# Performance work log

Hardware: AMD Instinct MI355X
Metric: run time of the kernel (lower is better)

The kernel has to match this reference:

```python
import jax, jax.numpy as jnp
import numpy as np

N_NODES = 100000
N_EDGES = 1600000
IN_CH = 128
OUT_CH = 128
BN_EPS = 1e-5


def setup_inputs() -> dict:
    key = jax.random.key(0)
    ks = jax.random.split(key, 8)
    x = jax.random.normal(ks[0], (N_NODES, IN_CH), dtype=jnp.float32)
    edge_index = jax.random.randint(ks[1], (2, N_EDGES), 0, N_NODES, dtype=jnp.int32)
    s1 = 1.0 / np.sqrt(IN_CH)
    s2 = 1.0 / np.sqrt(OUT_CH)
    W1 = jax.random.uniform(ks[2], (IN_CH, OUT_CH), minval=-s1, maxval=s1, dtype=jnp.float32)
    b1 = jax.random.uniform(ks[3], (OUT_CH,), minval=-s1, maxval=s1, dtype=jnp.float32)
    gamma = jnp.ones((OUT_CH,), dtype=jnp.float32)
    beta = jnp.zeros((OUT_CH,), dtype=jnp.float32)
    W2 = jax.random.uniform(ks[4], (OUT_CH, OUT_CH), minval=-s2, maxval=s2, dtype=jnp.float32)
    b2 = jax.random.uniform(ks[5], (OUT_CH,), minval=-s2, maxval=s2, dtype=jnp.float32)
    return {"x": x, "edge_index": edge_index, "W1": W1, "b1": b1,
            "gamma": gamma, "beta": beta, "W2": W2, "b2": b2}


def reference(x, edge_index, W1, b1, gamma, beta, W2, b2):
    # GINConv (eps=0): h_i = x_i + sum_{(j->i) in E} x_j
    src, dst = edge_index[0], edge_index[1]
    agg = jax.ops.segment_sum(x[src], dst, num_segments=N_NODES)  # [N, in_ch]
    h = x + agg
    # MLP: Linear -> BatchNorm1d (training-mode batch stats) -> ReLU -> Linear -> ReLU
    h = h @ W1 + b1                                   # [N, out_ch]
    mean = jnp.mean(h, axis=0)
    var = jnp.mean(jnp.square(h - mean), axis=0)      # biased variance, as in BN training
    h = (h - mean) * jax.lax.rsqrt(var + BN_EPS) * gamma + beta
    h = jax.nn.relu(h)
    h = h @ W2 + b2
    return jax.nn.relu(h)
```

## Files before the change

kernel.cpp:

```cpp
#include <hip/hip_runtime.h>
#include <hip/hip_bf16.h>
#include <hip/hip_fp16.h>
#include <stdint.h>

#define CH 128
#define NCHUNK 512
#define MAXBKT 2048

typedef _Float16 f16x8 __attribute__((ext_vector_type(8)));
typedef float f32x4 __attribute__((ext_vector_type(4)));

static __device__ __forceinline__ float4 ld4(const float* p) {
    return *reinterpret_cast<const float4*>(p);
}

static __device__ __forceinline__ void cvt_store_fp16(uint32_t* xh, int i, float4 v0, float4 v1) {
    __half2 h0 = __floats2half2_rn(v0.x, v0.y);
    __half2 h1 = __floats2half2_rn(v0.z, v0.w);
    __half2 h2 = __floats2half2_rn(v1.x, v1.y);
    __half2 h3 = __floats2half2_rn(v1.z, v1.w);
    uint4 o;
    o.x = *reinterpret_cast<unsigned*>(&h0);
    o.y = *reinterpret_cast<unsigned*>(&h1);
    o.z = *reinterpret_cast<unsigned*>(&h2);
    o.w = *reinterpret_cast<unsigned*>(&h3);
    reinterpret_cast<uint4*>(xh)[i] = o;
}

__global__ __launch_bounds__(256) void k_bhist_cvt(const float* __restrict__ x,
        uint32_t* __restrict__ xh, int n8, const int* __restrict__ dst,
        int* __restrict__ H, int nE, int nbkt, int chunkSz) {
    __shared__ int hist[MAXBKT];
    int c = blockIdx.x, tid = threadIdx.x;
    int gsz = gridDim.x * 256;
    for (int i = c * 256 + tid; i < n8; i += gsz)
        cvt_store_fp16(xh, i, ld4(x + (size_t)i * 8), ld4(x + (size_t)i * 8 + 4));
    for (int i = tid; i < nbkt; i += 256) hist[i] = 0;
    __syncthreads();
    int s = c * chunkSz, e = min(s + chunkSz, nE);
    for (int i = s + tid; i < e; i += 256) atomicAdd(&hist[dst[i] >> 6], 1);
    __syncthreads();
    for (int i = tid; i < nbkt; i += 256) H[c * nbkt + i] = hist[i];
}

__global__ void k_btot(const int* __restrict__ H, int* __restrict__ T, int nchunk, int nbkt) {
    __shared__ int sd[256];
    int b = blockIdx.x, tid = threadIdx.x;
    int v = 0;
    for (int c = tid; c < nchunk; c += 256) v += H[c * nbkt + b];
    sd[tid] = v;
    __syncthreads();
    for (int o = 128; o > 0; o >>= 1) {
        if (tid < o) sd[tid] += sd[tid + o];
        __syncthreads();
    }
    if (tid == 0) T[b] = sd[0];
}

__global__ __launch_bounds__(1024) void k_bscan(const int* __restrict__ T,
                                                int* __restrict__ base, int nbkt) {
    __shared__ int ps[1024];
    int t = threadIdx.x;
    int a0 = (2 * t < nbkt) ? T[2 * t] : 0;
    int a1 = (2 * t + 1 < nbkt) ? T[2 * t + 1] : 0;
    ps[t] = a0 + a1;
    __syncthreads();
    for (int d = 1; d < 1024; d <<= 1) {
        int v = (t >= d) ? ps[t - d] : 0;
        __syncthreads();
        ps[t] += v;
        __syncthreads();
    }
    int excl = t ? ps[t - 1] : 0;
    if (2 * t < nbkt) base[2 * t] = excl;
    if (2 * t + 1 < nbkt) base[2 * t + 1] = excl + a0;
    if (t == 0) base[nbkt] = ps[1023];
}

__global__ __launch_bounds__(512) void k_boff(int* H, const int* __restrict__ base,
                                              int nchunk, int nbkt) {
    __shared__ int sd[NCHUNK];
    int b = blockIdx.x, t = threadIdx.x;
    int v = (t < nchunk) ? H[t * nbkt + b] : 0;
    sd[t] = v;
    __syncthreads();
    for (int d = 1; d < NCHUNK; d <<= 1) {
        int tv = (t >= d) ? sd[t - d] : 0;
        __syncthreads();
        sd[t] += tv;
        __syncthreads();
    }
    if (t < nchunk) H[t * nbkt + b] = base[b] + sd[t] - v;
}

__global__ void k_bscatter(const int* __restrict__ src, const int* __restrict__ dst,
                           const int* __restrict__ H, int* __restrict__ sorted,
                           int nE, int nbkt, int chunkSz) {
    __shared__ int cur[MAXBKT];
    int c = blockIdx.x, tid = threadIdx.x;
    for (int i = tid; i < nbkt; i += 256) cur[i] = H[c * nbkt + i];
    __syncthreads();
    int s = c * chunkSz, e = min(s + chunkSz, nE);
    for (int i = s + tid; i < e; i += 256) {
        int d = dst[i];
        int pos = atomicAdd(&cur[d >> 6], 1);
        sorted[pos] = src[i] | ((d & 63) << 17);
    }
}

__global__ __launch_bounds__(256) void k_bsort2(const int* __restrict__ sorted,
        const int* __restrict__ base, int* __restrict__ csr, int* __restrict__ offs,
        int n, int nbkt, int nE) {
    __shared__ int hist[64];
    __shared__ int cur[64];
    int b = blockIdx.x, tid = threadIdx.x;
    if (tid < 64) hist[tid] = 0;
    __syncthreads();
    int s = base[b], e = base[b + 1];
    for (int i = s + tid; i < e; i += 256)
        atomicAdd(&hist[(sorted[i] >> 17) & 63], 1);
    __syncthreads();
    if (tid < 64) {
        int h0 = hist[tid], v = h0;
        for (int d = 1; d < 64; d <<= 1) {
            int t = __shfl_up(v, d, 64);
            if (tid >= d) v += t;
        }
        int excl = base[b] + v - h0;
        int node = b * 64 + tid;
        if (node < n) offs[node] = excl;
        cur[tid] = excl;
    }
    if (b == 0 && tid == 0) offs[n] = nE;
    __syncthreads();
    for (int i = s + tid; i < e; i += 256) {
        int p = sorted[i];
        int pos = atomicAdd(&cur[(p >> 17) & 63], 1);
        csr[pos] = (p & 0x1FFFF) << 5;
    }
}

static __device__ __forceinline__ void acc4(float4& a, uint2 v) {
    __half2 p0 = *reinterpret_cast<__half2*>(&v.x);
    __half2 p1 = *reinterpret_cast<__half2*>(&v.y);
    float2 f0 = __half22float2(p0), f1 = __half22float2(p1);
    a.x += f0.x; a.y += f0.y; a.z += f1.x; a.w += f1.y;
}

__global__ void k_aggregate_h2(const uint2* __restrict__ xv,
        const int* __restrict__ csr, const int* __restrict__ offs,
        uint2* __restrict__ h16, int n) {
    int wid = (blockIdx.x * blockDim.x + threadIdx.x) >> 6;
    int lane = threadIdx.x & 63;
    int nw = (gridDim.x * blockDim.x) >> 6;
    int hf = lane >> 5;
    int l32 = lane & 31;
    for (int node = wid; node < n; node += nw) {
        float4 a0 = make_float4(0.f, 0.f, 0.f, 0.f), a1 = a0, a2 = a0, a3 = a0;
        if (hf == 0) acc4(a0, xv[(size_t)node * 32 + l32]);
        int s = offs[node], e = offs[node + 1];
        int i = s + hf;
        for (; i + 14 < e; i += 16) {
            uint2 v0 = xv[csr[i]      + l32];
            uint2 v1 = xv[csr[i + 2]  + l32];
            uint2 v2 = xv[csr[i + 4]  + l32];
            uint2 v3 = xv[csr[i + 6]  + l32];
            uint2 v4 = xv[csr[i + 8]  + l32];
            uint2 v5 = xv[csr[i + 10] + l32];
            uint2 v6 = xv[csr[i + 12] + l32];
            uint2 v7 = xv[csr[i + 14] + l32];
            acc4(a0, v0); acc4(a1, v1); acc4(a2, v2); acc4(a3, v3);
            acc4(a0, v4); acc4(a1, v5); acc4(a2, v6); acc4(a3, v7);
        }
        for (; i + 6 < e; i += 8) {
            uint2 v0 = xv[csr[i]     + l32];
            uint2 v1 = xv[csr[i + 2] + l32];
            uint2 v2 = xv[csr[i + 4] + l32];
            uint2 v3 = xv[csr[i + 6] + l32];
            acc4(a0, v0); acc4(a1, v1); acc4(a2, v2); acc4(a3, v3);
        }
        for (; i < e; i += 2)
            acc4(a0, xv[csr[i] + l32]);
        a0.x += a1.x + a2.x + a3.x;
        a0.y += a1.y + a2.y + a3.y;
        a0.z += a1.z + a2.z + a3.z;
        a0.w += a1.w + a2.w + a3.w;
        a0.x += __shfl_xor(a0.x, 32, 64);
        a0.y += __shfl_xor(a0.y, 32, 64);
        a0.z += __shfl_xor(a0.z, 32, 64);
        a0.w += __shfl_xor(a0.w, 32, 64);
        if (hf == 0) {
            __half2 o0 = __floats2half2_rn(a0.x, a0.y);
            __half2 o1 = __floats2half2_rn(a0.z, a0.w);
            unsigned long long ov =
                (unsigned long long)(*reinterpret_cast<unsigned*>(&o0)) |
                ((unsigned long long)(*reinterpret_cast<unsigned*>(&o1)) << 32);
            __builtin_nontemporal_store(ov,
                reinterpret_cast<unsigned long long*>(&h16[(size_t)node * 32 + l32]));
        }
    }
}

__global__ __launch_bounds__(256) void k_mgemm(
        const _Float16* __restrict__ A, const float* __restrict__ W,
        const float* __restrict__ bias, _Float16* __restrict__ O16,
        float* __restrict__ O32, float* __restrict__ statsOut,
        const float* __restrict__ statsIn, const float* __restrict__ gamma,
        const float* __restrict__ beta, float invN, int nrows, int doStats) {
    __shared__ _Float16 WT[CH * CH];
    __shared__ float sc_sh[2 * CH];
    int tid = threadIdx.x;
    for (int idx4 = tid * 4; idx4 < CH * CH; idx4 += 1024) {
        float4 wv = ld4(W + idx4);
        int k = idx4 >> 7, col = idx4 & 127;
        int s = k >> 3, j = k & 7;
#pragma unroll
        for (int q = 0; q < 4; ++q) {
            int c = col + q;
            WT[c * CH + ((s ^ (c & 7)) << 3) + j] =
                (_Float16)(q == 0 ? wv.x : q == 1 ? wv.y : q == 2 ? wv.z : wv.w);
        }
    }
    if (statsIn && tid < CH) {
        float mean = statsIn[tid] * invN;
        float var = statsIn[CH + tid] * invN - mean * mean;
        float sc = gamma[tid] * rsqrtf(var + 1e-5f);
        sc_sh[tid] = sc;
        sc_sh[CH + tid] = beta[tid] - mean * sc;
    }
    __syncthreads();

    int wv = tid >> 6, lane = tid & 63;
    int lr = lane & 15;
    int lg = lane >> 4;

    float bv[8];
#pragma unroll
    for (int ct = 0; ct < 8; ++ct) bv[ct] = bias[ct * 16 + lr];
    float ssum[8], ssq[8];
#pragma unroll
    for (int ct = 0; ct < 8; ++ct) { ssum[ct] = 0.f; ssq[ct] = 0.f; }

    int nchunks = (nrows + 63) >> 6;
    for (int chunk = blockIdx.x; chunk < nchunks; chunk += gridDim.x) {
        int row0 = chunk * 64 + wv * 16;
        int arow = min(row0 + lr, nrows - 1);
        const _Float16* Ap = A + (size_t)arow * CH + lg * 8;
        f16x8 a[4];
#pragma unroll
        for (int kb = 0; kb < 4; ++kb)
            a[kb] = *reinterpret_cast<const f16x8*>(Ap + kb * 32);
        if (statsIn) {
#pragma unroll
            for (int kb = 0; kb < 4; ++kb) {
                int k0 = kb * 32 + lg * 8;
#pragma unroll
                for (int j = 0; j < 8; ++j) {
                    float f = (float)a[kb][j];
                    f = fmaxf(fmaf(f, sc_sh[k0 + j], sc_sh[CH + k0 + j]), 0.f);
                    a[kb][j] = (_Float16)f;
                }
            }
        }

        f32x4 acc[8];
#pragma unroll
        for (int ct = 0; ct < 8; ++ct) acc[ct] = (f32x4){0.f, 0.f, 0.f, 0.f};
#pragma unroll
        for (int ct = 0; ct < 8; ++ct) {
            int col = ct * 16 + lr;
            const _Float16* Wp = &WT[col * CH];
            int sw = (col & 7) << 3;
#pragma unroll
            for (int kb = 0; kb < 4; ++kb) {
                int s = kb * 4 + lg;
                f16x8 b = *reinterpret_cast<const f16x8*>(Wp + ((s << 3) ^ sw));
                acc[ct] = __builtin_amdgcn_mfma_f32_16x16x32_f16(a[kb], b, acc[ct], 0, 0, 0);
            }
        }

#pragma unroll
        for (int ct = 0; ct < 8; ++ct) {
            int col = ct * 16 + lr;
#pragma unroll
            for (int r = 0; r < 4; ++r) {
                int row = row0 + lg * 4 + r;
                if (row < nrows) {
                    float v = acc[ct][r] + bv[ct];
                    if (doStats) {
                        O16[(size_t)row * CH + col] = (_Float16)v;
                        ssum[ct] += v;
                        ssq[ct] += v * v;
                    } else {
                        O32[(size_t)row * CH + col] = fmaxf(v, 0.f);
                    }
                }
            }
        }
    }

    if (doStats) {
#pragma unroll
        for (int ct = 0; ct < 8; ++ct) {
            ssum[ct] += __shfl_xor(ssum[ct], 16, 64); ssum[ct] += __shfl_xor(ssum[ct], 32, 64);
            ssq[ct]  += __shfl_xor(ssq[ct], 16, 64);  ssq[ct]  += __shfl_xor(ssq[ct], 32, 64);
        }
        __syncthreads();
        float* red = (float*)WT;
        if (lg == 0) {
#pragma unroll
            for (int ct = 0; ct < 8; ++ct) {
                red[wv * 128 + ct * 16 + lr] = ssum[ct];
                red[512 + wv * 128 + ct * 16 + lr] = ssq[ct];
            }
        }
        __syncthreads();
        if (tid < 128) {
            float s = 0.f, q = 0.f;
#pragma unroll
            for (int w = 0; w < 4; ++w) { s += red[w * 128 + tid]; q += red[512 + w * 128 + tid]; }
            atomicAdd(&statsOut[tid], s);
            atomicAdd(&statsOut[128 + tid], q);
        }
    }
}

extern "C" void kernel_launch(void* const* d_in, const int* in_sizes, int n_in,
                              void* d_out, int out_size, void* d_ws, size_t ws_size,
                              hipStream_t stream) {
    const float* x     = (const float*)d_in[0];
    const int*   ei    = (const int*)d_in[1];
    const float* W1    = (const float*)d_in[2];
    const float* b1    = (const float*)d_in[3];
    const float* gamma = (const float*)d_in[4];
    const float* beta  = (const float*)d_in[5];
    const float* W2    = (const float*)d_in[6];
    const float* b2    = (const float*)d_in[7];

    int N = in_sizes[0] / CH;
    int E = in_sizes[1] / 2;
    const int* esrc = ei;
    const int* edst = ei + E;
    int nbkt = (N + 63) >> 6;
    int chunkSz = (E + NCHUNK - 1) / NCHUNK;
    int n8 = N * CH / 8;

    int* H      = (int*)d_out;
    int* sorted = (int*)((char*)d_out + (((size_t)NCHUNK * nbkt * 4 + 255) & ~(size_t)255));
    _Float16* h16 = (_Float16*)d_out;

    char* w = (char*)d_ws;
    auto take = [&](size_t bytes) {
        char* p = w;
        w += (bytes + 255) & ~(size_t)255;
        return p;
    };
    int*      csr    = (int*)take((size_t)E * 4);
    int*      T      = (int*)take((size_t)(nbkt + 1) * 4);
    int*      base   = (int*)take((size_t)(nbkt + 1) * 4);
    int*      offs   = (int*)take((size_t)(N + 1) * 4);
    float*    stats  = (float*)take(256 * 4);
    uint32_t* xh     = (uint32_t*)take((size_t)N * CH * 2);
    _Float16* h1     = (_Float16*)xh;

    (void)hipMemsetAsync(stats, 0, 256 * 4, stream);

    k_bhist_cvt<<<NCHUNK, 256, 0, stream>>>(x, xh, n8, edst, H, E, nbkt, chunkSz);
    k_btot<<<nbkt, 256, 0, stream>>>(H, T, NCHUNK, nbkt);
    k_bscan<<<1, 1024, 0, stream>>>(T, base, nbkt);
    k_boff<<<nbkt, NCHUNK, 0, stream>>>(H, base, NCHUNK, nbkt);
    k_bscatter<<<NCHUNK, 256, 0, stream>>>(esrc, edst, H, sorted, E, nbkt, chunkSz);
    k_bsort2<<<nbkt, 256, 0, stream>>>(sorted, base, csr, offs, N, nbkt, E);
    k_aggregate_h2<<<4096, 256, 0, stream>>>((const uint2*)xh, csr, offs,
                                             (uint2*)h16, N);
    k_mgemm<<<512, 256, 0, stream>>>(h16, W1, b1, h1, nullptr, stats,
                                     nullptr, nullptr, nullptr, 0.f, N, 1);
    k_mgemm<<<512, 256, 0, stream>>>(h1, W2, b2, nullptr, (float*)d_out, nullptr,
                                     stats, gamma, beta, 1.0f / (float)N, N, 0);
}
```

Before: 206.7 us.

## Slice fp16 node features into 8 channel slices mapped to XCDs for aggregation

Stores the fp16 copy of x as 8 separate channel slices of 16 channels each. Aggregation blocks are assigned one slice by blockIdx mod 8, and each node's slice is gathered by 4 threads. Because blocks are dispatched round-robin across XCDs, each XCD should gather only from a ~3.2 MB slice that can stay in its L2 instead of going to MALL or HBM. The trade-offs are that CSR indices are re-read once per slice, each gather is only 32 bytes, and the first GEMM must read its A operand from the sliced layout.

```diff
diff --git a/kernel.cpp b/kernel.cpp
--- a/kernel.cpp
+++ b/kernel.cpp
@@ -6,6 +6,7 @@
 #define CH 128
 #define NCHUNK 512
 #define MAXBKT 2048
+#define NSLICE 8
 
 typedef _Float16 f16x8 __attribute__((ext_vector_type(8)));
 typedef float f32x4 __attribute__((ext_vector_type(4)));
@@ -14,27 +15,31 @@
     return *reinterpret_cast<const float4*>(p);
 }
 
-static __device__ __forceinline__ void cvt_store_fp16(uint32_t* xh, int i, float4 v0, float4 v1) {
-    __half2 h0 = __floats2half2_rn(v0.x, v0.y);
-    __half2 h1 = __floats2half2_rn(v0.z, v0.w);
-    __half2 h2 = __floats2half2_rn(v1.x, v1.y);
-    __half2 h3 = __floats2half2_rn(v1.z, v1.w);
-    uint4 o;
-    o.x = *reinterpret_cast<unsigned*>(&h0);
-    o.y = *reinterpret_cast<unsigned*>(&h1);
-    o.z = *reinterpret_cast<unsigned*>(&h2);
-    o.w = *reinterpret_cast<unsigned*>(&h3);
-    reinterpret_cast<uint4*>(xh)[i] = o;
-}
-
 __global__ __launch_bounds__(256) void k_bhist_cvt(const float* __restrict__ x,
-        uint32_t* __restrict__ xh, int n8, const int* __restrict__ dst,
+        uint2* __restrict__ xh, int n, const int* __restrict__ dst,
         int* __restrict__ H, int nE, int nbkt, int chunkSz) {
     __shared__ int hist[MAXBKT];
     int c = blockIdx.x, tid = threadIdx.x;
     int gsz = gridDim.x * 256;
-    for (int i = c * 256 + tid; i < n8; i += gsz)
-        cvt_store_fp16(xh, i, ld4(x + (size_t)i * 8), ld4(x + (size_t)i * 8 + 4));
+    int nw = n * NSLICE;
+    for (int i = c * 256 + tid; i < nw; i += gsz) {
+        int node = i >> 3, s = i & 7;
+        const float* xp = x + (size_t)node * CH + s * 16;
+        float4 v0 = ld4(xp), v1 = ld4(xp + 4), v2 = ld4(xp + 8), v3 = ld4(xp + 12);
+        __half2 h0 = __floats2half2_rn(v0.x, v0.y);
+        __half2 h1 = __floats2half2_rn(v0.z, v0.w);
+        __half2 h2 = __floats2half2_rn(v1.x, v1.y);
+        __half2 h3 = __floats2half2_rn(v1.z, v1.w);
+        __half2 h4 = __floats2half2_rn(v2.x, v2.y);
+        __half2 h5 = __floats2half2_rn(v2.z, v2.w);
+        __half2 h6 = __floats2half2_rn(v3.x, v3.y);
+        __half2 h7 = __floats2half2_rn(v3.z, v3.w);
+        uint2* o = &xh[(size_t)s * n * 4 + (size_t)node * 4];
+        o[0] = make_uint2(*reinterpret_cast<unsigned*>(&h0), *reinterpret_cast<unsigned*>(&h1));
+        o[1] = make_uint2(*reinterpret_cast<unsigned*>(&h2), *reinterpret_cast<unsigned*>(&h3));
+        o[2] = make_uint2(*reinterpret_cast<unsigned*>(&h4), *reinterpret_cast<unsigned*>(&h5));
+        o[3] = make_uint2(*reinterpret_cast<unsigned*>(&h6), *reinterpret_cast<unsigned*>(&h7));
+    }
     for (int i = tid; i < nbkt; i += 256) hist[i] = 0;
     __syncthreads();
     int s = c * chunkSz, e = min(s + chunkSz, nE);
@@ -136,7 +141,7 @@
     for (int i = s + tid; i < e; i += 256) {
         int p = sorted[i];
         int pos = atomicAdd(&cur[(p >> 17) & 63], 1);
-        csr[pos] = (p & 0x1FFFF) << 5;
+        csr[pos] = (p & 0x1FFFF) << 2;
     }
 }
 
@@ -147,57 +152,48 @@
     a.x += f0.x; a.y += f0.y; a.z += f1.x; a.w += f1.y;
 }
 
-__global__ void k_aggregate_h2(const uint2* __restrict__ xv,
+__global__ __launch_bounds__(256) void k_aggregate_s(const uint2* __restrict__ xv,
         const int* __restrict__ csr, const int* __restrict__ offs,
         uint2* __restrict__ h16, int n) {
-    int wid = (blockIdx.x * blockDim.x + threadIdx.x) >> 6;
-    int lane = threadIdx.x & 63;
-    int nw = (gridDim.x * blockDim.x) >> 6;
-    int hf = lane >> 5;
-    int l32 = lane & 31;
-    for (int node = wid; node < n; node += nw) {
-        float4 a0 = make_float4(0.f, 0.f, 0.f, 0.f), a1 = a0, a2 = a0, a3 = a0;
-        if (hf == 0) acc4(a0, xv[(size_t)node * 32 + l32]);
-        int s = offs[node], e = offs[node + 1];
-        int i = s + hf;
-        for (; i + 14 < e; i += 16) {
-            uint2 v0 = xv[csr[i]      + l32];
-            uint2 v1 = xv[csr[i + 2]  + l32];
-            uint2 v2 = xv[csr[i + 4]  + l32];
-            uint2 v3 = xv[csr[i + 6]  + l32];
-            uint2 v4 = xv[csr[i + 8]  + l32];
-            uint2 v5 = xv[csr[i + 10] + l32];
-            uint2 v6 = xv[csr[i + 12] + l32];
-            uint2 v7 = xv[csr[i + 14] + l32];
-            acc4(a0, v0); acc4(a1, v1); acc4(a2, v2); acc4(a3, v3);
-            acc4(a0, v4); acc4(a1, v5); acc4(a2, v6); acc4(a3, v7);
-        }
-        for (; i + 6 < e; i += 8) {
-            uint2 v0 = xv[csr[i]     + l32];
-            uint2 v1 = xv[csr[i + 2] + l32];
-            uint2 v2 = xv[csr[i + 4] + l32];
-            uint2 v3 = xv[csr[i + 6] + l32];
-            acc4(a0, v0); acc4(a1, v1); acc4(a2, v2); acc4(a3, v3);
-        }
-        for (; i < e; i += 2)
-            acc4(a0, xv[csr[i] + l32]);
-        a0.x += a1.x + a2.x + a3.x;
-        a0.y += a1.y + a2.y + a3.y;
-        a0.z += a1.z + a2.z + a3.z;
-        a0.w += a1.w + a2.w + a3.w;
-        a0.x += __shfl_xor(a0.x, 32, 64);
-        a0.y += __shfl_xor(a0.y, 32, 64);
-        a0.z += __shfl_xor(a0.z, 32, 64);
-        a0.w += __shfl_xor(a0.w, 32, 64);
-        if (hf == 0) {
-            __half2 o0 = __floats2half2_rn(a0.x, a0.y);
-            __half2 o1 = __floats2half2_rn(a0.z, a0.w);
-            unsigned long long ov =
-                (unsigned long long)(*reinterpret_cast<unsigned*>(&o0)) |
-                ((unsigned long long)(*reinterpret_cast<unsigned*>(&o1)) << 32);
-            __builtin_nontemporal_store(ov,
-                reinterpret_cast<unsigned long long*>(&h16[(size_t)node * 32 + l32]));
-        }
+    int s = blockIdx.x & (NSLICE - 1);
+    int blk = blockIdx.x >> 3;
+    int nblk = gridDim.x >> 3;
+    int tid = threadIdx.x;
+    int g = tid >> 2;
+    int c = tid & 3;
+    size_t sb = (size_t)s * n * 4;
+
+    int chunk = (n + nblk - 1) / nblk;
+    int node0 = blk * chunk;
+    int node1 = min(node0 + chunk, n);
+
+    for (int node = node0 + g; node < node1; node += 64) {
+        float4 a0, a1 = make_float4(0.f, 0.f, 0.f, 0.f);
+        {
+            uint2 v = xv[sb + (size_t)node * 4 + c];
+            __half2 p0 = *reinterpret_cast<__half2*>(&v.x);
+            __half2 p1 = *reinterpret_cast<__half2*>(&v.y);
+            float2 f0 = __half22float2(p0), f1 = __half22float2(p1);
+            a0 = make_float4(f0.x, f0.y, f1.x, f1.y);
+        }
+        int i = offs[node], e = offs[node + 1];
+        for (; i + 3 < e; i += 4) {
+            uint2 v0 = xv[sb + csr[i] + c];
+            uint2 v1 = xv[sb + csr[i + 1] + c];
+            uint2 v2 = xv[sb + csr[i + 2] + c];
+            uint2 v3 = xv[sb + csr[i + 3] + c];
+            acc4(a0, v0); acc4(a1, v1); acc4(a0, v2); acc4(a1, v3);
+        }
+        for (; i < e; ++i)
+            acc4(a0, xv[sb + csr[i] + c]);
+        a0.x += a1.x; a0.y += a1.y; a0.z += a1.z; a0.w += a1.w;
+        __half2 o0 = __floats2half2_rn(a0.x, a0.y);
+        __half2 o1 = __floats2half2_rn(a0.z, a0.w);
+        unsigned long long ov =
+            (unsigned long long)(*reinterpret_cast<unsigned*>(&o0)) |
+            ((unsigned long long)(*reinterpret_cast<unsigned*>(&o1)) << 32);
+        __builtin_nontemporal_store(ov,
+            reinterpret_cast<unsigned long long*>(&h16[sb + (size_t)node * 4 + c]));
     }
 }
 
@@ -206,7 +202,7 @@
         const float* __restrict__ bias, _Float16* __restrict__ O16,
         float* __restrict__ O32, float* __restrict__ statsOut,
         const float* __restrict__ statsIn, const float* __restrict__ gamma,
-        const float* __restrict__ beta, float invN, int nrows, int doStats) {
+        const float* __restrict__ beta, float invN, int nrows, int doStats, int aSliced) {
     __shared__ _Float16 WT[CH * CH];
     __shared__ float sc_sh[2 * CH];
     int tid = threadIdx.x;
@@ -245,11 +241,20 @@
     for (int chunk = blockIdx.x; chunk < nchunks; chunk += gridDim.x) {
         int row0 = chunk * 64 + wv * 16;
         int arow = min(row0 + lr, nrows - 1);
-        const _Float16* Ap = A + (size_t)arow * CH + lg * 8;
         f16x8 a[4];
-#pragma unroll
-        for (int kb = 0; kb < 4; ++kb)
-            a[kb] = *reinterpret_cast<const f16x8*>(Ap + kb * 32);
+        if (aSliced) {
+#pragma unroll
+            for (int kb = 0; kb < 4; ++kb) {
+                int s = kb * 2 + (lg >> 1);
+                a[kb] = *reinterpret_cast<const f16x8*>(
+                    A + (size_t)s * nrows * 16 + (size_t)arow * 16 + (lg & 1) * 8);
+            }
+        } else {
+            const _Float16* Ap = A + (size_t)arow * CH + lg * 8;
+#pragma unroll
+            for (int kb = 0; kb < 4; ++kb)
+                a[kb] = *reinterpret_cast<const f16x8*>(Ap + kb * 32);
+        }
         if (statsIn) {
 #pragma unroll
             for (int kb = 0; kb < 4; ++kb) {
@@ -343,7 +348,6 @@
     const int* edst = ei + E;
     int nbkt = (N + 63) >> 6;
     int chunkSz = (E + NCHUNK - 1) / NCHUNK;
-    int n8 = N * CH / 8;
 
     int* H      = (int*)d_out;
     int* sorted = (int*)((char*)d_out + (((size_t)NCHUNK * nbkt * 4 + 255) & ~(size_t)255));
@@ -360,21 +364,20 @@
     int*      base   = (int*)take((size_t)(nbkt + 1) * 4);
     int*      offs   = (int*)take((size_t)(N + 1) * 4);
     float*    stats  = (float*)take(256 * 4);
-    uint32_t* xh     = (uint32_t*)take((size_t)N * CH * 2);
+    uint2*    xh     = (uint2*)take((size_t)N * CH * 2);
     _Float16* h1     = (_Float16*)xh;
 
     (void)hipMemsetAsync(stats, 0, 256 * 4, stream);
 
-    k_bhist_cvt<<<NCHUNK, 256, 0, stream>>>(x, xh, n8, edst, H, E, nbkt, chunkSz);
+    k_bhist_cvt<<<NCHUNK, 256, 0, stream>>>(x, xh, N, edst, H, E, nbkt, chunkSz);
     k_btot<<<nbkt, 256, 0, stream>>>(H, T, NCHUNK, nbkt);
     k_bscan<<<1, 1024, 0, stream>>>(T, base, nbkt);
     k_boff<<<nbkt, NCHUNK, 0, stream>>>(H, base, NCHUNK, nbkt);
     k_bscatter<<<NCHUNK, 256, 0, stream>>>(esrc, edst, H, sorted, E, nbkt, chunkSz);
     k_bsort2<<<nbkt, 256, 0, stream>>>(sorted, base, csr, offs, N, nbkt, E);
-    k_aggregate_h2<<<4096, 256, 0, stream>>>((const uint2*)xh, csr, offs,
-                                             (uint2*)h16, N);
+    k_aggregate_s<<<2048, 256, 0, stream>>>(xh, csr, offs, (uint2*)h16, N);
     k_mgemm<<<512, 256, 0, stream>>>(h16, W1, b1, h1, nullptr, stats,
-                                     nullptr, nullptr, nullptr, 0.f, N, 1);
+                                     nullptr, nullptr, nullptr, 0.f, N, 1, 1);
     k_mgemm<<<512, 256, 0, stream>>>(h1, W2, b2, nullptr, (float*)d_out, nullptr,
-                                     stats, gamma, beta, 1.0f / (float)N, N, 0);
-}
+                                     stats, gamma, beta, 1.0f / (float)N, N, 0, 0);
+}
```

New measurement: 231.1 us. 1.12x slower.
